# Optimization experiments

Hardware: AMD Instinct MI355X
Metric: run time of the kernel (lower is better)

The kernel has to match this reference:

```python
import jax, jax.numpy as jnp
import numpy as np
from jax import lax

B, L, D, H = 48, 512, 384, 384


def setup_inputs() -> dict:
    key = jax.random.key(0)
    ks = jax.random.split(key, 8)
    def w(k, shape, fan):
        return jax.random.normal(k, shape, jnp.float32) / np.float32(np.sqrt(fan))
    return {
        "v": jax.random.normal(ks[0], (B, L, D), jnp.float32),
        "mask": jnp.ones((B, L), jnp.bool_),
        "Wp_cur": w(ks[1], (D, H), D),      # torch Wp (applied to v_i)
        "Wp_seq": w(ks[2], (D, H), D),      # torch Wp_ (applied to all of v)
        "V": w(ks[3], (H,), H),             # torch V: Linear(H, 1, bias=False)
        "W_ih": w(ks[4], (3 * H, 2 * D), 2 * D),  # GRUCell input weights
        "W_hh": w(ks[5], (3 * H, H), H),           # GRUCell hidden weights
        "b_ih": jnp.zeros((3 * H,), jnp.float32),
        "b_hh": jnp.zeros((3 * H,), jnp.float32),
    }


def _forward(v, mask, Wp_cur, Wp_seq, V, W_ih, W_hh, b_ih, b_hh):
    Bv, Lv, _ = v.shape
    Hh = W_hh.shape[1]
    # Torch recomputes Wp_(v) identically every step; hoist it (same math).
    Wpv = jnp.einsum('bld,dh->blh', v, Wp_seq)            # [B,L,H]
    neg = jnp.where(mask, 0.0, -1e30).astype(v.dtype)     # additive attention mask [B,L]

    def step(h, vi):                                       # vi: [B,D], h: [B,H]
        wpi = vi @ Wp_cur                                  # [B,H]
        x = jnp.tanh(Wpv + wpi[:, None, :])                # [B,L,H]
        s = jnp.einsum('blh,h->bl', x, V) + neg            # scores [B,L]
        a = jax.nn.softmax(s, axis=1)                      # masked softmax
        c = jnp.einsum('bl,bld->bd', a, v)                 # context [B,D]
        r = jnp.concatenate([vi, c], axis=1)               # [B,2D]
        gi = r @ W_ih.T + b_ih
        gh = h @ W_hh.T + b_hh
        ir, iz, inn = jnp.split(gi, 3, axis=1)
        hr, hz, hn = jnp.split(gh, 3, axis=1)
        rg = jax.nn.sigmoid(ir + hr)
        zg = jax.nn.sigmoid(iz + hz)
        ng = jnp.tanh(inn + rg * hn)
        hnew = (1.0 - zg) * ng + zg * h                    # PyTorch GRUCell update
        return hnew, hnew

    h0 = jnp.zeros((Bv, Hh), v.dtype)
    h_last, hs = lax.scan(jax.checkpoint(step), h0, jnp.swapaxes(v, 0, 1))
    hs = jnp.swapaxes(hs, 0, 1)                            # [B,L,H]
    # dropout p=0.0 -> identity; h = hs[:, -1]
    return hs, h_last


def reference(v, mask, Wp_cur, Wp_seq, V, W_ih, W_hh, b_ih, b_hh):
    return _forward(v, mask, Wp_cur, Wp_seq, V, W_ih, W_hh, b_ih, b_hh)
```

## Files before the change

kernel.cpp:

```cpp
#include <hip/hip_runtime.h>


typedef unsigned short u16;
typedef unsigned int u32;
typedef short short8 __attribute__((ext_vector_type(8)));
typedef float f32x4 __attribute__((ext_vector_type(4)));
typedef float f4 __attribute__((ext_vector_type(4)));
typedef _Float16 h2_t __attribute__((ext_vector_type(2)));
typedef _Float16 h8_t __attribute__((ext_vector_type(8)));

#define BDIM 48
#define LDIM 512
#define DDIM 384
#define HDIM 384

__device__ __forceinline__ float bf2f(u16 u) { return __uint_as_float(((u32)u) << 16); }
__device__ __forceinline__ u16 f2bf(float f) {
  u32 x = __float_as_uint(f);
  u32 r = (x + 0x7fffu + ((x >> 16) & 1u)) >> 16;
  return (u16)r;
}
__device__ __forceinline__ float h16f(u16 u) {
  union { u16 u; _Float16 h; } c; c.u = u; return (float)c.h;
}
__device__ __forceinline__ float sigm(float x) {
  return __builtin_amdgcn_rcpf(1.f + exp2f(-1.4426950408889634f * x));
}
__device__ __forceinline__ float tanh_f(float x) {
  float e = exp2f(2.885390081777927f * x);
  return 1.f - 2.f * __builtin_amdgcn_rcpf(e + 1.f);
}

__device__ __forceinline__ u32 load_sc0(const u32* p) {
  u32 v;
  asm volatile("global_load_dword %0, %1, off sc0\n\ts_waitcnt vmcnt(0)"
               : "=v"(v) : "v"(p) : "memory");
  return v;
}
__device__ __forceinline__ u32 load_sc01(const u32* p) {
  u32 v;
  asm volatile("global_load_dword %0, %1, off sc0 sc1\n\ts_waitcnt vmcnt(0)"
               : "=v"(v) : "v"(p) : "memory");
  return v;
}
__device__ __forceinline__ void store_sc01(u32* p, u32 v) {
  asm volatile("global_store_dword %0, %1, off sc0 sc1" :: "v"(p), "v"(v) : "memory");
}

__device__ __forceinline__ void load16(const void* src, long ld, int isf32,
                                       long row, int kbase, short8& o0, short8& o1)
{
  if (isf32) {
    const float* s = (const float*)src + row * ld + kbase;
    f4 q0 = *(const f4*)(s);
    f4 q1 = *(const f4*)(s + 4);
    f4 q2 = *(const f4*)(s + 8);
    f4 q3 = *(const f4*)(s + 12);
    short8 a, b;
    a[0] = (short)f2bf(q0[0]); a[1] = (short)f2bf(q0[1]);
    a[2] = (short)f2bf(q0[2]); a[3] = (short)f2bf(q0[3]);
    a[4] = (short)f2bf(q1[0]); a[5] = (short)f2bf(q1[1]);
    a[6] = (short)f2bf(q1[2]); a[7] = (short)f2bf(q1[3]);
    b[0] = (short)f2bf(q2[0]); b[1] = (short)f2bf(q2[1]);
    b[2] = (short)f2bf(q2[2]); b[3] = (short)f2bf(q2[3]);
    b[4] = (short)f2bf(q3[0]); b[5] = (short)f2bf(q3[1]);
    b[6] = (short)f2bf(q3[2]); b[7] = (short)f2bf(q3[3]);
    o0 = a; o1 = b;
  } else {
    const u16* s = (const u16*)src + row * ld + kbase;
    o0 = *(const short8*)s;
    o1 = *(const short8*)(s + 8);
  }
}

__global__ __launch_bounds__(256) void gemm_bt(
    const void* __restrict__ A1, const void* __restrict__ A2,
    long lda1, long lda2, int ksplit, int a1f, int a2f,
    const void* __restrict__ Bm, long ldb, int bfm,
    u16* __restrict__ Out, int N, int K,
    long strideA, long strideB, long strideO,
    const float* __restrict__ bias, int epi_exp2, int out_bf16)
{
  __shared__ u16 As[128][40];
  __shared__ u16 Bs[128][40];
  const int tid = threadIdx.x;
  const int lane = tid & 63;
  const int w = tid >> 6;
  const int wm = w >> 1, wn = w & 1;
  const int l15 = lane & 15, quad = lane >> 4;
  const long m0 = (long)blockIdx.x * 128;
  const long n0 = (long)blockIdx.y * 128;
  const int z = blockIdx.z;
  const char* A1p = (const char*)A1 + (long)z * strideA * (a1f ? 4 : 2);
  const char* A2p = (const char*)A2 + (long)z * strideA * (a2f ? 4 : 2);
  const char* Bp  = (const char*)Bm + (long)z * strideB * (bfm ? 4 : 2);
  u16* Op = Out + (long)z * strideO;

  const int r2 = tid & 127;
  const int half = tid >> 7;

  f32x4 acc[4][4];
#pragma unroll
  for (int a = 0; a < 4; a++)
#pragma unroll
    for (int c = 0; c < 4; c++) acc[a][c] = (f32x4){0.f, 0.f, 0.f, 0.f};

  for (int k0 = 0; k0 < K; k0 += 32) {
    const void* srcA; long lda; int kk; int af;
    if (k0 < ksplit) { srcA = A1p; lda = lda1; kk = k0; af = a1f; }
    else             { srcA = A2p; lda = lda2; kk = k0 - ksplit; af = a2f; }
    short8 a0, a1, b0, b1;
    load16(srcA, lda, af, m0 + r2, kk + half * 16, a0, a1);
    load16(Bp, ldb, bfm, n0 + r2, k0 + half * 16, b0, b1);
    __syncthreads();
    *(short8*)&As[r2][half * 16] = a0;
    *(short8*)&As[r2][half * 16 + 8] = a1;
    *(short8*)&Bs[r2][half * 16] = b0;
    *(short8*)&Bs[r2][half * 16 + 8] = b1;
    __syncthreads();
    short8 af_[4], bf_[4];
#pragma unroll
    for (int mt = 0; mt < 4; mt++) af_[mt] = *(const short8*)&As[wm * 64 + mt * 16 + l15][quad * 8];
#pragma unroll
    for (int nt = 0; nt < 4; nt++) bf_[nt] = *(const short8*)&Bs[wn * 64 + nt * 16 + l15][quad * 8];
#pragma unroll
    for (int mt = 0; mt < 4; mt++)
#pragma unroll
      for (int nt = 0; nt < 4; nt++)
        acc[mt][nt] = __builtin_amdgcn_mfma_f32_16x16x32_bf16(af_[mt], bf_[nt], acc[mt][nt], 0, 0, 0);
  }

#pragma unroll
  for (int mt = 0; mt < 4; mt++) {
#pragma unroll
    for (int nt = 0; nt < 4; nt++) {
      const long col = n0 + wn * 64 + nt * 16 + l15;
      float bv = bias ? bias[col] : 0.f;
#pragma unroll
      for (int rg = 0; rg < 4; rg++) {
        long row = m0 + wm * 64 + mt * 16 + quad * 4 + rg;
        float vv = acc[mt][nt][rg] + bv;
        if (epi_exp2) {
          float t = vv * 2.885390081777927f;
          t = fminf(fmaxf(t, -15.9f), 15.9f);
          vv = exp2f(t);
        }
        long idx = row * (long)N + col;
        if (out_bf16) Op[idx] = f2bf(vv);
        else ((_Float16*)Op)[idx] = (_Float16)vv;
      }
    }
  }
}

__global__ void transpose_f2b(const float* __restrict__ src, u16* __restrict__ dst,
                              int rows, int cols, long sstride, long dstride)
{
  __shared__ float t[32][33];
  const int bz = blockIdx.z;
  const float* s = src + (long)bz * sstride;
  u16* d = dst + (long)bz * dstride;
  const int c0 = blockIdx.x * 32, r0 = blockIdx.y * 32;
  const int tx = threadIdx.x, ty = threadIdx.y;
#pragma unroll
  for (int j = 0; j < 4; j++) t[ty + j * 8][tx] = s[(long)(r0 + ty + j * 8) * cols + c0 + tx];
  __syncthreads();
#pragma unroll
  for (int j = 0; j < 4; j++) d[(long)(c0 + ty + j * 8) * rows + r0 + tx] = f2bf(t[tx][ty + j * 8]);
}

__global__ __launch_bounds__(256) void attn_softmax(
    const _Float16* __restrict__ E, const _Float16* __restrict__ F,
    const float* __restrict__ Vw, u16* __restrict__ Aout)
{
  const int blk = blockIdx.x;
  const int x8 = blk & 7;
  const int rest = blk >> 3;
  const int ig = rest & 127;
  const int b = x8 + 8 * (rest >> 7);
  const int i0 = ig * 4;
  const int tid = threadIdx.x;
  const int lane = tid & 63, w = tid >> 6;
  const int r = lane & 15, sub = lane >> 4;
  __shared__ float Tl[4][512];

  float fv[4][24], vv[24];
#pragma unroll
  for (int ii = 0; ii < 4; ii++) {
    const h8_t* Fr = (const h8_t*)(F + ((long)b * LDIM + i0 + ii) * HDIM + r * 24);
    h8_t q0 = Fr[0], q1 = Fr[1], q2 = Fr[2];
#pragma unroll
    for (int j = 0; j < 8; j++) {
      fv[ii][j] = (float)q0[j]; fv[ii][8 + j] = (float)q1[j]; fv[ii][16 + j] = (float)q2[j];
    }
  }
  const float* Vp = Vw + r * 24;
#pragma unroll
  for (int j = 0; j < 24; j++) vv[j] = Vp[j];

  for (int li = 0; li < 32; ++li) {
    const int l = li * 16 + w * 4 + sub;
    const h8_t* Er = (const h8_t*)(E + ((long)b * LDIM + l) * HDIM + r * 24);
    h8_t e0 = Er[0], e1 = Er[1], e2 = Er[2];
    float ev[24];
#pragma unroll
    for (int j = 0; j < 8; j++) {
      ev[j] = (float)e0[j]; ev[8 + j] = (float)e1[j]; ev[16 + j] = (float)e2[j];
    }
    float p[4] = {0.f, 0.f, 0.f, 0.f};
#pragma unroll
    for (int j = 0; j < 24; j++) {
#pragma unroll
      for (int ii = 0; ii < 4; ii++)
        p[ii] += vv[j] * __builtin_amdgcn_rcpf(ev[j] * fv[ii][j] + 1.f);
    }
#pragma unroll
    for (int ii = 0; ii < 4; ii++) {
      float q = p[ii];
      q += __shfl_xor(q, 1);
      q += __shfl_xor(q, 2);
      q += __shfl_xor(q, 4);
      q += __shfl_xor(q, 8);
      if (r == 0) Tl[ii][l] = q;
    }
  }
  __syncthreads();

  float t[8];
  float mn = 1e30f;
#pragma unroll
  for (int k = 0; k < 8; k++) { t[k] = Tl[w][lane + 64 * k]; mn = fminf(mn, t[k]); }
#pragma unroll
  for (int off = 32; off; off >>= 1) mn = fminf(mn, __shfl_xor(mn, off));
  const float C2 = 2.885390081777927f;
  float p8[8], Z = 0.f;
#pragma unroll
  for (int k = 0; k < 8; k++) { p8[k] = exp2f(C2 * (mn - t[k])); Z += p8[k]; }
#pragma unroll
  for (int off = 32; off; off >>= 1) Z += __shfl_xor(Z, off);
  const float inv = __builtin_amdgcn_rcpf(Z);
  u16* Ar = Aout + ((long)b * LDIM + i0 + w) * LDIM;
#pragma unroll
  for (int k = 0; k < 8; k++) Ar[lane + 64 * k] = f2bf(p8[k] * inv);
}

__global__ __launch_bounds__(512, 2) void recurrence(
    const float* __restrict__ Whh, const float* __restrict__ bhh_g,
    const u16* __restrict__ GIu, u32* __restrict__ hslots,
    float* __restrict__ out)
{
  const int blk = blockIdx.x;
  const int x8 = blk & 7;
  const int s = blk >> 3;
  const int b = x8 + 8 * (s % 6);
  const int g = s / 6;
  const int tid = threadIdx.x;
  const int tx = tid & 15;
  const int ty = tid >> 4;

  __shared__ _Float16 hall[HDIM];
  __shared__ float gh[288];

  h2_t wv[9][12];
  float bh[9];
#pragma unroll
  for (int q = 0; q < 9; q++) {
    int rr = ty * 9 + q;
    int R = (rr / 96) * 384 + g * 96 + (rr % 96);
    const f4* wq = (const f4*)(Whh + (long)R * HDIM + tx * 24);
#pragma unroll
    for (int t6 = 0; t6 < 6; t6++) {
      f4 u = wq[t6];
      wv[q][2 * t6]     = (h2_t){(_Float16)u[0], (_Float16)u[1]};
      wv[q][2 * t6 + 1] = (h2_t){(_Float16)u[2], (_Float16)u[3]};
    }
    bh[q] = (tx == 0) ? bhh_g[R] : 0.f;
  }

  if (tid < HDIM) hall[tid] = (_Float16)0.f;
  __syncthreads();

  const long gi_base = (long)b * LDIM * 1152;
  float hprev = 0.f;
  u16 c0 = 0, c1 = 0, c2 = 0;
  if (tid < 96) {
    const long gb = gi_base + g * 96 + tid;
    c0 = GIu[gb]; c1 = GIu[gb + 384]; c2 = GIu[gb + 768];
  }

  for (int i = 0; i < LDIM; ++i) {
    if (i > 0) {
      if (tid < HDIM && (tid / 96) != g) {
        u32* slot = hslots + (long)(i & 1) * (BDIM * HDIM) + (long)b * HDIM + tid;
        u32 val;
        int n = 0;
        for (;;) {
          val = ((n & 3) == 3) ? load_sc01(slot) : load_sc0(slot);
          if ((val >> 16) == (u32)i) break;
          ++n;
        }
        union { u16 u; _Float16 h; } cv;
        cv.u = (u16)val;
        hall[tid] = cv.h;
      }
      __syncthreads();
    }

    u16 n0 = 0, n1 = 0, n2 = 0;
    if (tid < 96 && i + 1 < LDIM) {
      const long gb = gi_base + (long)(i + 1) * 1152 + g * 96 + tid;
      n0 = GIu[gb]; n1 = GIu[gb + 384]; n2 = GIu[gb + 768];
    }

    h2_t hv[12];
#pragma unroll
    for (int p = 0; p < 12; p++) hv[p] = *(const h2_t*)&hall[tx * 24 + 2 * p];
    float ac[9];
#pragma unroll
    for (int q = 0; q < 9; q++) {
      float a = 0.f;
#pragma unroll
      for (int p = 0; p < 12; p++) a = __builtin_amdgcn_fdot2(wv[q][p], hv[p], a, false);
      ac[q] = a;
    }
#pragma unroll
    for (int q = 0; q < 9; q++) {
      float a = ac[q];
      a += __shfl_xor(a, 1);
      a += __shfl_xor(a, 2);
      a += __shfl_xor(a, 4);
      a += __shfl_xor(a, 8);
      if (tx == 0) gh[ty * 9 + q] = a + bh[q];
    }
    __syncthreads();
    if (tid < 96) {
      const int j = g * 96 + tid;
      float hr = gh[tid], hz = gh[96 + tid], hn = gh[192 + tid];
      float rg = sigm(h16f(c0) + hr);
      float zg = sigm(h16f(c1) + hz);
      float ng = tanh_f(h16f(c2) + rg * hn);
      float hnew = (1.f - zg) * ng + zg * hprev;
      hprev = hnew;
      union { _Float16 h; u16 u; } cv;
      cv.h = (_Float16)hnew;
      if (i + 1 < LDIM) {
        const u32 val = ((u32)(i + 1) << 16) | (u32)cv.u;
        store_sc01(hslots + (long)((i + 1) & 1) * (BDIM * HDIM) + (long)b * HDIM + j, val);
      }
      hall[j] = cv.h;
      out[((long)b * LDIM + i) * HDIM + j] = hnew;
      if (i == LDIM - 1) out[(long)BDIM * LDIM * HDIM + (long)b * HDIM + j] = hnew;
    }
    c0 = n0; c1 = n1; c2 = n2;
  }
}

extern "C" void kernel_launch(void* const* d_in, const int* in_sizes, int n_in,
                              void* d_out, int out_size, void* d_ws, size_t ws_size,
                              hipStream_t stream)
{
  (void)in_sizes; (void)n_in; (void)out_size; (void)ws_size;
  const float* v      = (const float*)d_in[0];
  const float* Wp_cur = (const float*)d_in[2];
  const float* Wp_seq = (const float*)d_in[3];
  const float* Vw     = (const float*)d_in[4];
  const float* W_ih   = (const float*)d_in[5];
  const float* W_hh   = (const float*)d_in[6];
  const float* b_ih   = (const float*)d_in[7];
  const float* b_hh   = (const float*)d_in[8];
  float* out = (float*)d_out;

  char* ws = (char*)d_ws;
  size_t off = 0;
  auto alloc = [&](size_t bytes) -> char* {
    char* p = ws + off;
    off += (bytes + 255) & ~(size_t)255;
    return p;
  };
  u32* hslots = (u32*)alloc((size_t)2 * 48 * 384 * 4);
  u16* WpSeqT = (u16*)alloc((size_t)384 * 384 * 2);
  u16* WpCurT = (u16*)alloc((size_t)384 * 384 * 2);
  u16* Cbuf   = (u16*)alloc((size_t)24576 * 384 * 2);
  u16* vT     = (u16*)alloc((size_t)48 * 384 * 512 * 2);
  char* region = alloc((size_t)24576 * 384 * 2 * 2 + (size_t)24576 * 512 * 2);
  _Float16* E  = (_Float16*)region;
  _Float16* F  = (_Float16*)(region + (size_t)24576 * 384 * 2);
  u16* Abuf    = (u16*)(region + (size_t)24576 * 384 * 2 * 2);
  _Float16* GI = (_Float16*)region;

  transpose_f2b<<<dim3(12, 12, 1), dim3(32, 8), 0, stream>>>(Wp_seq, WpSeqT, 384, 384, 0, 0);
  transpose_f2b<<<dim3(12, 12, 1), dim3(32, 8), 0, stream>>>(Wp_cur, WpCurT, 384, 384, 0, 0);
  transpose_f2b<<<dim3(12, 16, 48), dim3(32, 8), 0, stream>>>(v, vT, 512, 384,
                                                              (long)512 * 384, (long)384 * 512);

  gemm_bt<<<dim3(192, 3, 1), 256, 0, stream>>>(v, v, 384, 384, 1 << 30, 1, 1,
                                               WpSeqT, 384, 0,
                                               (u16*)E, 384, 384, 0, 0, 0, nullptr, 1, 0);
  gemm_bt<<<dim3(192, 3, 1), 256, 0, stream>>>(v, v, 384, 384, 1 << 30, 1, 1,
                                               WpCurT, 384, 0,
                                               (u16*)F, 384, 384, 0, 0, 0, nullptr, 1, 0);

  attn_softmax<<<dim3(6144), 256, 0, stream>>>(E, F, Vw, Abuf);

  gemm_bt<<<dim3(4, 3, 48), 256, 0, stream>>>(Abuf, Abuf, 512, 512, 1 << 30, 0, 0,
                                              vT, 512, 0,
                                              Cbuf, 384, 512,
                                              (long)512 * 512, (long)384 * 512, (long)512 * 384,
                                              nullptr, 0, 1);

  gemm_bt<<<dim3(192, 9, 1), 256, 0, stream>>>(v, Cbuf, 384, 384, 384, 1, 0,
                                               W_ih, 768, 1,
                                               (u16*)GI, 1152, 768, 0, 0, 0, b_ih, 0, 0);

  void* args[] = {(void*)&W_hh, (void*)&b_hh, (void*)&GI, (void*)&hslots, (void*)&out};
  hipLaunchCooperativeKernel(recurrence, dim3(192), dim3(512), args, 0, stream);
}
```

Baseline: 2.469 ms.

## Add probed fast-path h exchange through non-system-coherent slots in recurrence

The recurrence now publishes each new hidden value twice: a plain store to a fast slot array and a system-scope store to a slow one. At startup, the four blocks that share a batch row run a handshake to test whether a plain store from a peer is visible through an sc0 load (same XCD/L2). If it is, consumers poll the fast slot and check the slow slot every eighth iteration, so a missed or stale fast copy still gets caught. The aim is to cut per-step cross-block sync latency by avoiding sc1 (system-coherent) loads, at the cost of an extra store per element and a heuristic visibility probe.

Measured after the change: 2.356 ms. 4.6% less time.

```diff
diff --git a/kernel.cpp b/kernel.cpp
--- a/kernel.cpp
+++ b/kernel.cpp
@@ -31,6 +31,12 @@
   return 1.f - 2.f * __builtin_amdgcn_rcpf(e + 1.f);
 }
 
+__device__ __forceinline__ void store_plain(u32* p, u32 v) {
+  asm volatile("global_store_dword %0, %1, off" :: "v"(p), "v"(v) : "memory");
+}
+__device__ __forceinline__ void store_sc01(u32* p, u32 v) {
+  asm volatile("global_store_dword %0, %1, off sc0 sc1" :: "v"(p), "v"(v) : "memory");
+}
 __device__ __forceinline__ u32 load_sc0(const u32* p) {
   u32 v;
   asm volatile("global_load_dword %0, %1, off sc0\n\ts_waitcnt vmcnt(0)"
@@ -42,9 +48,6 @@
   asm volatile("global_load_dword %0, %1, off sc0 sc1\n\ts_waitcnt vmcnt(0)"
                : "=v"(v) : "v"(p) : "memory");
   return v;
-}
-__device__ __forceinline__ void store_sc01(u32* p, u32 v) {
-  asm volatile("global_store_dword %0, %1, off sc0 sc1" :: "v"(p), "v"(v) : "memory");
 }
 
 __device__ __forceinline__ void load16(const void* src, long ld, int isf32,
@@ -246,7 +249,8 @@
 
 __global__ __launch_bounds__(512, 2) void recurrence(
     const float* __restrict__ Whh, const float* __restrict__ bhh_g,
-    const u16* __restrict__ GIu, u32* __restrict__ hslots,
+    const u16* __restrict__ GIu, u32* __restrict__ hfast,
+    u32* __restrict__ hslow, u32* __restrict__ pfast, u32* __restrict__ prdy,
     float* __restrict__ out)
 {
   const int blk = blockIdx.x;
@@ -260,6 +264,7 @@
 
   __shared__ _Float16 hall[HDIM];
   __shared__ float gh[288];
+  __shared__ int sx[4];
 
   h2_t wv[9][12];
   float bh[9];
@@ -278,7 +283,24 @@
   }
 
   if (tid < HDIM) hall[tid] = (_Float16)0.f;
+
+  if (tid == 0) {
+    store_plain(pfast + b * 4 + g, 0x5A5A0000u | (u32)g);
+    asm volatile("s_waitcnt vmcnt(0)" ::: "memory");
+    store_sc01(prdy + b * 4 + g, 0x5A5A0000u | (u32)g);
+  }
+  if (tid < 4 && tid != g) {
+    while (load_sc01(prdy + b * 4 + tid) != (0x5A5A0000u | (u32)tid)) {}
+  }
   __syncthreads();
+  if (tid < 4) {
+    sx[tid] = (tid != g) &&
+              (load_sc0(pfast + b * 4 + tid) == (0x5A5A0000u | (u32)tid));
+  }
+  __syncthreads();
+
+  const int pg = tid / 96;
+  int fastok = (tid < HDIM && pg != g) ? sx[pg] : 0;
 
   const long gi_base = (long)b * LDIM * 1152;
   float hprev = 0.f;
@@ -290,14 +312,22 @@
 
   for (int i = 0; i < LDIM; ++i) {
     if (i > 0) {
-      if (tid < HDIM && (tid / 96) != g) {
-        u32* slot = hslots + (long)(i & 1) * (BDIM * HDIM) + (long)b * HDIM + tid;
+      if (tid < HDIM && pg != g) {
+        const long soff = (long)(i & 1) * (BDIM * HDIM) + (long)b * HDIM + tid;
         u32 val;
-        int n = 0;
-        for (;;) {
-          val = ((n & 3) == 3) ? load_sc01(slot) : load_sc0(slot);
-          if ((val >> 16) == (u32)i) break;
-          ++n;
+        if (fastok) {
+          int n = 0;
+          for (;;) {
+            if ((n & 7) == 7) {
+              val = load_sc01(hslow + soff);
+              if ((val >> 16) == (u32)i) { fastok = 0; break; }
+            }
+            val = load_sc0(hfast + soff);
+            if ((val >> 16) == (u32)i) break;
+            ++n;
+          }
+        } else {
+          do { val = load_sc01(hslow + soff); } while ((val >> 16) != (u32)i);
         }
         union { u16 u; _Float16 h; } cv;
         cv.u = (u16)val;
@@ -345,7 +375,9 @@
       cv.h = (_Float16)hnew;
       if (i + 1 < LDIM) {
         const u32 val = ((u32)(i + 1) << 16) | (u32)cv.u;
-        store_sc01(hslots + (long)((i + 1) & 1) * (BDIM * HDIM) + (long)b * HDIM + j, val);
+        const long soff = (long)((i + 1) & 1) * (BDIM * HDIM) + (long)b * HDIM + j;
+        store_plain(hfast + soff, val);
+        store_sc01(hslow + soff, val);
       }
       hall[j] = cv.h;
       out[((long)b * LDIM + i) * HDIM + j] = hnew;
@@ -377,7 +409,10 @@
     off += (bytes + 255) & ~(size_t)255;
     return p;
   };
-  u32* hslots = (u32*)alloc((size_t)2 * 48 * 384 * 4);
+  u32* hfast  = (u32*)alloc((size_t)2 * 48 * 384 * 4);
+  u32* hslow  = (u32*)alloc((size_t)2 * 48 * 384 * 4);
+  u32* pfast  = (u32*)alloc((size_t)48 * 4 * 4);
+  u32* prdy   = (u32*)alloc((size_t)48 * 4 * 4);
   u16* WpSeqT = (u16*)alloc((size_t)384 * 384 * 2);
   u16* WpCurT = (u16*)alloc((size_t)384 * 384 * 2);
   u16* Cbuf   = (u16*)alloc((size_t)24576 * 384 * 2);
@@ -412,6 +447,7 @@
                                                W_ih, 768, 1,
                                                (u16*)GI, 1152, 768, 0, 0, 0, b_ih, 0, 0);
 
-  void* args[] = {(void*)&W_hh, (void*)&b_hh, (void*)&GI, (void*)&hslots, (void*)&out};
+  void* args[] = {(void*)&W_hh, (void*)&b_hh, (void*)&GI, (void*)&hfast,
+                  (void*)&hslow, (void*)&pfast, (void*)&prdy, (void*)&out};
   hipLaunchCooperativeKernel(recurrence, dim3(192), dim3(512), args, 0, stream);
 }
```
